# Kernel optimization log

Measured on AMD Instinct MI355X. Metric: run time of the kernel, lower is better.

The kernel has to match this reference:

```python
import jax, jax.numpy as jnp
import numpy as np

N = 5
C = 256
B, H, W = 8, 64, 64


def setup_inputs() -> dict:
    key = jax.random.key(0)
    ks = jax.random.split(key, 9)
    s = 0.05
    return {
        "inputs": jax.random.normal(ks[0], (B, N, C, H, W), dtype=jnp.float32),
        # grouped 1x1 conv: groups = N-1, each group maps C channels -> 1 channel, no bias
        "wgt_w": jax.random.normal(ks[1], (N - 1, C), dtype=jnp.float32) * s,
        # ConvGRU 1x1 gate convs: in = 2*C (cat of input and hidden), out = C, with bias
        "w_r": jax.random.normal(ks[2], (C, 2 * C), dtype=jnp.float32) * s,
        "b_r": jnp.zeros((C,), dtype=jnp.float32),
        "w_u": jax.random.normal(ks[3], (C, 2 * C), dtype=jnp.float32) * s,
        "b_u": jnp.zeros((C,), dtype=jnp.float32),
        "w_o": jax.random.normal(ks[4], (C, 2 * C), dtype=jnp.float32) * s,
        "b_o": jnp.zeros((C,), dtype=jnp.float32),
        "gamma": jax.random.normal(ks[5], (1,), dtype=jnp.float32) * s,
    }


def _conv1x1(x, Wm, bias):
    # x: [b, cin, h, w]; Wm: [cout, cin]
    return jnp.einsum("bchw,oc->bohw", x, Wm) + bias[None, :, None, None]


def reference(inputs, wgt_w, w_r, b_r, w_u, b_u, w_o, b_o, gamma):
    b, n, c, h, w = inputs.shape

    def gru(x, hprev):
        s = jnp.concatenate([x, hprev], axis=1)  # [b, 2c, h, w]
        u = jax.nn.sigmoid(_conv1x1(s, w_u, b_u))
        r = jax.nn.sigmoid(_conv1x1(s, w_r, b_r))
        o = jnp.tanh(_conv1x1(jnp.concatenate([x, hprev * r], axis=1), w_o, b_o))
        return hprev * (1.0 - u) + o * u

    preds = []
    for i in range(n):
        h_t = inputs[:, i]  # [b, c, h, w]
        idx = [j for j in range(n) if j != i]
        h_n = inputs[:, jnp.array(idx)]  # [b, n-1, c, h, w], neighbor-major channel layout
        diff = h_t[:, None] - h_n  # repeat(h_t, n-1) - cat(neighbors)
        # grouped 1x1 conv (groups = n-1, no bias): per-neighbor channel reduction
        wgt = jnp.einsum("bjchw,jc->bjhw", diff, wgt_w)  # [b, n-1, h, w]
        gate = jax.nn.sigmoid(wgt)
        # torch: wgt.unsqueeze(1).repeat(1, c, 1, 1, 1).view(b, c*(n-1), h, w)
        # -> flat channel index = cc*(n-1) + j  (note: differs from x2's j*c + cc layout)
        gate_full = jnp.broadcast_to(gate[:, None], (b, c, n - 1, h, w)).reshape(
            b, c * (n - 1), h, w
        )
        x2 = h_n.reshape(b, (n - 1) * c, h, w)
        msg = x2 * gate_full
        m_t = msg.reshape(b, n - 1, c, h, w).sum(axis=1)  # sum-aggregate over neighbors
        h_new = gru(m_t, h_t)
        preds.append(h_new * gamma + h_t)
    return jnp.stack(preds, axis=1)  # [b, n, c, h, w]
```

## Files before the change

kernel.cpp:

```cpp
#include <hip/hip_runtime.h>

typedef __attribute__((ext_vector_type(8))) short short8;
typedef __attribute__((ext_vector_type(4))) float f32x4;
typedef __attribute__((ext_vector_type(8))) unsigned short us8;
typedef __attribute__((ext_vector_type(4))) unsigned short us4;
typedef __attribute__((ext_vector_type(2))) unsigned short us2;

__device__ __forceinline__ float sigmoidf_(float x){ return 1.f/(1.f+__expf(-x)); }
__device__ __forceinline__ unsigned short f2bf(float f){
    union{float f; unsigned int u;} x; x.f = f;
    unsigned int r = x.u + 0x7fffu + ((x.u>>16)&1u);
    return (unsigned short)(r>>16);
}
__device__ __forceinline__ float bf2f(unsigned short u){
    union{unsigned int u; float f;} x; x.u = ((unsigned int)u)<<16; return x.f;
}
#define GAS(p) ((const __attribute__((address_space(1))) void*)(uintptr_t)(p))
#define LAS(p) ((__attribute__((address_space(3))) void*)(uintptr_t)(p))

#define SLOT 8388608ull

__global__ __launch_bounds__(256) void k_dots(const float* __restrict__ inp, const float* __restrict__ wgt,
                                              float* __restrict__ D){
    __shared__ float wg[1024];
    for (int s=threadIdx.x; s<1024; s+=256) wg[s] = wgt[s];
    __syncthreads();
    int e = blockIdx.x*256 + threadIdx.x;
    int pl = e & 4095;
    int bn = e >> 12;
    const float* base = inp + (((size_t)bn*256)<<12) + pl;
    float d0=0,d1=0,d2=0,d3=0;
    #pragma unroll 8
    for (int c=0;c<256;c++){
        float v = base[(size_t)c<<12];
        d0 += v*wg[c]; d1 += v*wg[256+c]; d2 += v*wg[512+c]; d3 += v*wg[768+c];
    }
    size_t o = ((size_t)bn*4)<<12;
    D[o+pl]=d0; D[o+4096+pl]=d1; D[o+8192+pl]=d2; D[o+12288+pl]=d3;
}

__global__ __launch_bounds__(256) void k_wp2(const float* __restrict__ w_u, const float* __restrict__ w_r,
                                             const float* __restrict__ w_o,
                                             unsigned short* __restrict__ Wc0, unsigned short* __restrict__ Wc1){
    int bx = blockIdx.x;
    const float *s0, *s1; unsigned short* dst; int OCN, tid;
    if (bx < 256){ tid = bx*256 + threadIdx.x; OCN = 512; s0 = w_u; s1 = w_r; dst = Wc0; }
    else         { tid = (bx-256)*256 + threadIdx.x; OCN = 256; s0 = w_o; s1 = w_o; dst = Wc1; }
    int d = tid*4;
    int kk = d & 63;
    int row = d >> 6;
    int oc = row & (OCN-1);
    int kb = row / OCN;
    int k  = kb*64 + kk;
    const float* src = (oc < 256) ? s0 : s1;
    int ocr = (oc < 256) ? oc : oc-256;
    float4 v = *(const float4*)&src[(size_t)ocr*512 + k];
    us4 pk; pk.x=f2bf(v.x); pk.y=f2bf(v.y); pk.z=f2bf(v.z); pk.w=f2bf(v.w);
    int kk_sw = kk ^ ((oc&7)<<3);
    *(us4*)&dst[(size_t)row*64 + kk_sw] = pk;
}

__global__ __launch_bounds__(256) void k_bxs(const float* __restrict__ inp, const float* __restrict__ D,
                                             unsigned short* __restrict__ Alo, unsigned short* __restrict__ Ahi,
                                             int i0, int cnt){
    __shared__ unsigned short tm[64*34];
    __shared__ unsigned short th[64*34];
    int t  = threadIdx.x;
    int c0 = (blockIdx.x & 3) << 6;
    int pz = blockIdx.x >> 2;
    int p0 = pz << 5;
    int b  = p0 >> 12, pl0 = p0 & 4095;

    f32x4 x[5][2], S4[2];
    #pragma unroll
    for (int q=0;q<2;q++){
        int s = t + q*256;
        int c = s >> 3, pc = (s&7) << 2;
        int cc = c0 + c;
        f32x4 acc = {0.f,0.f,0.f,0.f};
        #pragma unroll
        for (int n=0;n<5;n++){
            x[n][q] = *(const f32x4*)&inp[(((size_t)((b*5+n)*256+cc))<<12) + pl0 + pc];
            acc += x[n][q];
        }
        S4[q] = acc;
    }
    int kb = c0 >> 6;
    #pragma unroll
    for (int i=0;i<5;i++){
        if (i < i0 || i >= i0+cnt) continue;
        #pragma unroll
        for (int q=0;q<2;q++){
            int s = t + q*256;
            int c = s >> 3, pc = (s&7) << 2;
            int j = c & 3;
            int node = (j < i) ? j : (j+1);
            f32x4 dw = *(const f32x4*)&D[(((size_t)((b*5+i)*4+j))<<12) + pl0 + pc];
            f32x4 dn = *(const f32x4*)&D[(((size_t)((b*5+node)*4+j))<<12) + pl0 + pc];
            f32x4 xi = x[i][q];
            f32x4 md = S4[q] - xi;
            int lb = c*34 + pc;
            us2 m0, m1, h0, h1;
            m0.x = f2bf(sigmoidf_(dw.x-dn.x)*md.x); m0.y = f2bf(sigmoidf_(dw.y-dn.y)*md.y);
            m1.x = f2bf(sigmoidf_(dw.z-dn.z)*md.z); m1.y = f2bf(sigmoidf_(dw.w-dn.w)*md.w);
            h0.x = f2bf(xi.x); h0.y = f2bf(xi.y); h1.x = f2bf(xi.z); h1.y = f2bf(xi.w);
            *(us2*)&tm[lb] = m0; *(us2*)&tm[lb+2] = m1;
            *(us2*)&th[lb] = h0; *(us2*)&th[lb+2] = h1;
        }
        __syncthreads();
        {
            int p = t >> 3, cs = (t&7) << 3;
            us8 vm, vh;
            #pragma unroll
            for (int j8=0;j8<8;j8++){ vm[j8] = tm[(cs+j8)*34 + p]; vh[j8] = th[(cs+j8)*34 + p]; }
            int cs_sw = cs ^ ((p&7)<<3);
            size_t dst = (size_t)(i - i0)*SLOT + ((size_t)kb*32768 + p0 + p)*64 + cs_sw;
            *(us8*)&Alo[dst] = vm;
            *(us8*)&Ahi[dst] = vh;
        }
        __syncthreads();
    }
}

template<int EPI>
__global__ __launch_bounds__(256) void k_mm(
        const unsigned short* __restrict__ Alo, const unsigned short* __restrict__ Ahi,
        const unsigned short* __restrict__ Wb,
        const float* __restrict__ inp, const float* __restrict__ b0, const float* __restrict__ b1,
        unsigned short* __restrict__ U, unsigned short* __restrict__ A1hi, float* __restrict__ outp,
        const float* __restrict__ gamma_p, int i0)
{
    constexpr int OCN = EPI ? 256 : 512;
    constexpr int NY  = EPI ? 2   : 4;
    constexpr int NWG = 256*NY;
    __shared__ unsigned short As[2][128*64];
    __shared__ unsigned short Bs[2][128*64];
    int t  = threadIdx.x, wv = t>>6, ln = t&63;

    int bid = blockIdx.x;
    int wg  = (bid&7)*(NWG>>3) + (bid>>3);
    int oc0 = (wg & (NY-1)) * 128;
    int p0  = (wg / NY) * 128;

    int z  = blockIdx.z, i = i0 + z;
    size_t zo = (size_t)z*SLOT;
    int wm = (wv>>1)*64, wn = (wv&1)*64;
    int row = ln & 15, quad = ln >> 4, kq = quad*8;

    f32x4 acc[4][4];
    f32x4 zr = {0.f,0.f,0.f,0.f};
    #pragma unroll
    for (int a=0;a<4;a++){
        #pragma unroll
        for (int o=0;o<4;o++) acc[a][o]=zr;
    }

    auto stage = [&](int kb, int buf){
        const unsigned short* gA = (kb<4) ? (Alo + zo + ((size_t)kb*32768 + p0)*64)
                                          : (Ahi + zo + ((size_t)(kb-4)*32768 + p0)*64);
        const unsigned short* gW = Wb + ((size_t)kb*OCN + oc0)*64;
        #pragma unroll
        for (int q=0;q<4;q++){
            int off = (wv*4+q)*512;
            __builtin_amdgcn_global_load_lds(GAS(gA + off + ln*8), LAS(&Bs[buf][off + ln*8]), 16, 0, 0);
            __builtin_amdgcn_global_load_lds(GAS(gW + off + ln*8), LAS(&As[buf][off + ln*8]), 16, 0, 0);
        }
    };

    stage(0, 0);
    __syncthreads();

    int rsw = (row&7)<<3;
    for (int kb=0; kb<8; ++kb){
        int cur = kb & 1;
        if (kb < 7) stage(kb+1, cur^1);
        #pragma unroll
        for (int ks=0; ks<2; ks++){
            short8 a[4], b[4];
            int col = (ks*32 + kq) ^ rsw;
            #pragma unroll
            for (int f=0; f<4; f++){
                a[f] = *(const short8*)&As[cur][(wm+f*16+row)*64 + col];
                b[f] = *(const short8*)&Bs[cur][(wn+f*16+row)*64 + col];
            }
            __builtin_amdgcn_s_setprio(1);
            #pragma unroll
            for (int fm=0; fm<4; fm++){
                #pragma unroll
                for (int fn=0; fn<4; fn++)
                    acc[fm][fn] = __builtin_amdgcn_mfma_f32_16x16x32_bf16(a[fm], b[fn], acc[fm][fn], 0,0,0);
            }
            __builtin_amdgcn_s_setprio(0);
        }
        __syncthreads();
    }

    float gm = EPI ? gamma_p[0] : 0.f;
    #pragma unroll
    for (int fn=0; fn<4; fn++){
        int p  = p0 + wn + fn*16 + row;
        int b  = p >> 12, pl = p & 4095;
        size_t hb = (((size_t)((b*5+i)*256))<<12) + pl;
        #pragma unroll
        for (int fm=0; fm<4; fm++){
            int ocb = oc0 + wm + fm*16 + quad*4;
            if (EPI==0){
                if (oc0 < 256){
                    us4 pk;
                    #pragma unroll
                    for (int r=0;r<4;r++)
                        pk[r] = f2bf(sigmoidf_(acc[fm][fn][r] + b0[ocb+r]));
                    *(us4*)&U[zo + (size_t)p*256 + ocb] = pk;
                } else {
                    int kb2 = ocb - 256;
                    int kc  = (kb2&63) ^ ((p&7)<<3);
                    size_t aidx = zo + ((size_t)(kb2>>6)*32768 + p)*64 + kc;
                    us4 vh = *(const us4*)&Ahi[aidx];
                    us4 pk;
                    #pragma unroll
                    for (int r=0;r<4;r++){
                        float rg = sigmoidf_(acc[fm][fn][r] + b1[kb2+r]);
                        pk[r] = f2bf(rg * bf2f(vh[r]));
                    }
                    *(us4*)&A1hi[aidx] = pk;
                }
            } else {
                us4 vu = *(const us4*)&U[zo + (size_t)p*256 + ocb];
                #pragma unroll
                for (int r=0;r<4;r++){
                    int oc = ocb + r;
                    float v  = acc[fm][fn][r] + b0[oc];
                    float e2 = __expf(2.f*v);
                    float thv = 1.f - 2.f/(e2+1.f);
                    float u  = bf2f(vu[r]);
                    float h  = inp[hb + ((size_t)oc<<12)];
                    float hn = h*(1.f-u) + thv*u;
                    outp[hb + ((size_t)oc<<12)] = hn*gm + h;
                }
            }
        }
    }
}

extern "C" void kernel_launch(void* const* d_in, const int* in_sizes, int n_in,
                              void* d_out, int out_size, void* d_ws, size_t ws_size,
                              hipStream_t stream) {
    const float* inputs = (const float*)d_in[0];
    const float* wgt_w  = (const float*)d_in[1];
    const float* w_r    = (const float*)d_in[2];
    const float* b_r    = (const float*)d_in[3];
    const float* w_u    = (const float*)d_in[4];
    const float* b_u    = (const float*)d_in[5];
    const float* w_o    = (const float*)d_in[6];
    const float* b_o    = (const float*)d_in[7];
    const float* gamma  = (const float*)d_in[8];
    float* out = (float*)d_out;

    float* D = (float*)d_ws;
    unsigned short* Wc0 = (unsigned short*)(D + 655360);
    unsigned short* Wc1 = Wc0 + 262144;
    unsigned short* U   = Wc1 + 131072;

    size_t fixedB = 655360ull*4 + (262144ull + 131072ull)*2;
    size_t slotB  = 4ull*SLOT*2;
    int nb = 1;
    for (int k2=5;k2>=1;k2--){ if (fixedB + (size_t)k2*slotB <= ws_size){ nb = k2; break; } }

    unsigned short* Alo  = U   + (size_t)nb*SLOT;
    unsigned short* Ahi  = Alo + (size_t)nb*SLOT;
    unsigned short* A1hi = Ahi + (size_t)nb*SLOT;

    k_dots<<<640, 256, 0, stream>>>(inputs, wgt_w, D);
    k_wp2 <<<384, 256, 0, stream>>>(w_u, w_r, w_o, Wc0, Wc1);
    for (int i0=0; i0<5; i0+=nb){
        int cnt = (5-i0 < nb) ? (5-i0) : nb;
        k_bxs<<<4096, 256, 0, stream>>>(inputs, D, Alo, Ahi, i0, cnt);
        k_mm<0><<<dim3(1024,1,cnt), 256, 0, stream>>>(Alo, Ahi, Wc0, inputs, b_u, b_r,
                                                      U, A1hi, nullptr, gamma, i0);
        k_mm<1><<<dim3(512,1,cnt), 256, 0, stream>>>(Alo, A1hi, Wc1, inputs, b_o, nullptr,
                                                     U, nullptr, out, gamma, i0);
    }
}
```

Before: 707.6 us.

## Deepen GEMM pipeline to 4 LDS stages and restructure epilogue stores

Measured after the change: 718.9 us. No clear change (+1.6%).

```diff
diff --git a/kernel.cpp b/kernel.cpp
--- a/kernel.cpp
+++ b/kernel.cpp
@@ -133,8 +133,8 @@
     constexpr int OCN = EPI ? 256 : 512;
     constexpr int NY  = EPI ? 2   : 4;
     constexpr int NWG = 256*NY;
-    __shared__ unsigned short As[2][128*64];
-    __shared__ unsigned short Bs[2][128*64];
+    __shared__ unsigned short As[4][128*64];
+    __shared__ unsigned short Bs[4][128*64];
     int t  = threadIdx.x, wv = t>>6, ln = t&63;
 
     int bid = blockIdx.x;
@@ -167,13 +167,18 @@
         }
     };
 
-    stage(0, 0);
-    __syncthreads();
+    stage(0, 0); stage(1, 1); stage(2, 2);
 
     int rsw = (row&7)<<3;
+    #pragma unroll
     for (int kb=0; kb<8; ++kb){
-        int cur = kb & 1;
-        if (kb < 7) stage(kb+1, cur^1);
+        if (kb < 6)       { asm volatile("s_waitcnt vmcnt(16)" ::: "memory"); }
+        else if (kb == 6) { asm volatile("s_waitcnt vmcnt(8)"  ::: "memory"); }
+        else              { asm volatile("s_waitcnt vmcnt(0)"  ::: "memory"); }
+        __builtin_amdgcn_s_barrier();
+        __builtin_amdgcn_sched_barrier(0);
+        if (kb < 5) stage(kb+3, (kb+3)&3);
+        const int cur = kb & 3;
         #pragma unroll
         for (int ks=0; ks<2; ks++){
             short8 a[4], b[4];
@@ -192,40 +197,69 @@
             }
             __builtin_amdgcn_s_setprio(0);
         }
-        __syncthreads();
-    }
-
-    float gm = EPI ? gamma_p[0] : 0.f;
-    #pragma unroll
-    for (int fn=0; fn<4; fn++){
-        int p  = p0 + wn + fn*16 + row;
-        int b  = p >> 12, pl = p & 4095;
-        size_t hb = (((size_t)((b*5+i)*256))<<12) + pl;
-        #pragma unroll
-        for (int fm=0; fm<4; fm++){
-            int ocb = oc0 + wm + fm*16 + quad*4;
-            if (EPI==0){
-                if (oc0 < 256){
+    }
+
+    if (EPI==0){
+        if (oc0 < 256){
+            size_t ub = zo + (size_t)((p0>>7)*2 + (oc0>>7))*16384 + (size_t)t*4;
+            #pragma unroll
+            for (int fn=0; fn<4; fn++){
+                #pragma unroll
+                for (int fm=0; fm<4; fm++){
+                    int ocb = oc0 + wm + fm*16 + quad*4;
                     us4 pk;
                     #pragma unroll
                     for (int r=0;r<4;r++)
                         pk[r] = f2bf(sigmoidf_(acc[fm][fn][r] + b0[ocb+r]));
-                    *(us4*)&U[zo + (size_t)p*256 + ocb] = pk;
-                } else {
-                    int kb2 = ocb - 256;
-                    int kc  = (kb2&63) ^ ((p&7)<<3);
-                    size_t aidx = zo + ((size_t)(kb2>>6)*32768 + p)*64 + kc;
-                    us4 vh = *(const us4*)&Ahi[aidx];
+                    *(us4*)&U[ub + (size_t)(fn*4+fm)*1024] = pk;
+                }
+            }
+        } else {
+            __syncthreads();
+            unsigned short* tr = &As[0][0];
+            int hb2 = (oc0-256)>>6;
+            #pragma unroll
+            for (int fn=0; fn<4; fn++){
+                int pl_ = wn + fn*16 + row;
+                int psw = (pl_&7)<<3;
+                #pragma unroll
+                for (int fm=0; fm<4; fm++){
+                    int lc = wm + fm*16 + quad*4;
+                    us4 vh = *(const us4*)&Bs[hb2 + (lc>>6)][pl_*64 + ((lc&63)^psw)];
                     us4 pk;
                     #pragma unroll
                     for (int r=0;r<4;r++){
-                        float rg = sigmoidf_(acc[fm][fn][r] + b1[kb2+r]);
+                        float rg = sigmoidf_(acc[fm][fn][r] + b1[(oc0-256)+lc+r]);
                         pk[r] = f2bf(rg * bf2f(vh[r]));
                     }
-                    *(us4*)&A1hi[aidx] = pk;
+                    *(us4*)&tr[pl_*136 + lc] = pk;
                 }
-            } else {
-                us4 vu = *(const us4*)&U[zo + (size_t)p*256 + ocb];
+            }
+            __syncthreads();
+            #pragma unroll
+            for (int j=0;j<8;j++){
+                int id = j*256 + t;
+                int p  = id >> 4;
+                int ch = id & 15;
+                int gp = p0 + p;
+                int gc = (oc0-256) + ch*8;
+                us8 v = *(const us8*)&tr[p*136 + ch*8];
+                size_t dst = zo + ((size_t)(gc>>6)*32768 + gp)*64 + ((gc&63)^((gp&7)<<3));
+                *(us8*)&A1hi[dst] = v;
+            }
+        }
+    } else {
+        float gm = gamma_p[0];
+        size_t ub = zo + (size_t)((p0>>7)*2 + (oc0>>7))*16384 + (size_t)t*4;
+        #pragma unroll
+        for (int fn=0; fn<4; fn++){
+            int p  = p0 + wn + fn*16 + row;
+            int b  = p >> 12, pl = p & 4095;
+            size_t hb = (((size_t)((b*5+i)*256))<<12) + pl;
+            #pragma unroll
+            for (int fm=0; fm<4; fm++){
+                int ocb = oc0 + wm + fm*16 + quad*4;
+                us4 vu = *(const us4*)&U[ub + (size_t)(fn*4+fm)*1024];
                 #pragma unroll
                 for (int r=0;r<4;r++){
                     int oc = ocb + r;
```
